# Kernel tuning notes

Hardware: AMD Instinct MI355X
Metric: run time of the kernel (lower is better)

The kernel has to match this reference:

```python
import jax, jax.numpy as jnp
import numpy as np
from itertools import permutations

NODE, BATCH, DIM, STEP = 32, 64, 32, 8
E = NODE * (NODE - 1)          # 992 directed edges (all ordered pairs)
K = 3                          # edge types
MSG_HID = 64; MSG_OUT = 64; N_HID = 64; PRED_LEN = 8


def setup_inputs() -> dict:
    key = jax.random.key(0)
    ks = jax.random.split(key, 12)
    es = jnp.asarray(np.array(list(permutations(range(NODE), 2))).T, dtype=jnp.int32)  # [2, E]
    x = jax.random.normal(ks[0], (BATCH, NODE, DIM, STEP), jnp.float32)
    z = jax.nn.softmax(jax.random.normal(ks[1], (BATCH, E, K), jnp.float32), axis=-1)
    p = lambda k, shape: jax.random.normal(k, shape, jnp.float32) * 0.1
    return dict(
        x=x, z=z, es=es,
        nodes_mask=jnp.zeros((NODE,), jnp.float32),
        edges_mask=jnp.zeros((E,), jnp.float32),
        mask=jnp.zeros((1,), jnp.float32),
        msg_W1=p(ks[2], (K, 2 * DIM, MSG_HID)), msg_b1=jnp.zeros((K, MSG_HID), jnp.float32),
        msg_W2=p(ks[3], (K, MSG_HID, MSG_OUT)), msg_b2=jnp.zeros((K, MSG_OUT), jnp.float32),
        out_W1=p(ks[4], (DIM + MSG_OUT, N_HID)), out_b1=jnp.zeros((N_HID,), jnp.float32),
        out_W2=p(ks[5], (N_HID, N_HID)), out_b2=jnp.zeros((N_HID,), jnp.float32),
        out_W3=p(ks[6], (N_HID, DIM)), out_b3=jnp.zeros((DIM,), jnp.float32),
        ge_Wi=p(ks[7], (3, N_HID, N_HID)), ge_bi=jnp.zeros((3, N_HID), jnp.float32),
        ge_Wh=p(ks[8], (3, N_HID, N_HID)), ge_bh=jnp.zeros((3, N_HID), jnp.float32),
        gn_Wi=p(ks[9], (3, N_HID + DIM, N_HID + DIM)), gn_bi=jnp.zeros((3, N_HID + DIM), jnp.float32),
        gn_Wh=p(ks[10], (3, N_HID + DIM, N_HID + DIM)), gn_bh=jnp.zeros((3, N_HID + DIM), jnp.float32),
    )


def _gru(inp, hid, Wi, bi, Wh, bh):
    # GRUX: state defaults to hidden
    r = jax.nn.sigmoid(inp @ Wi[0] + bi[0] + hid @ Wh[0] + bh[0])
    i = jax.nn.sigmoid(inp @ Wi[1] + bi[1] + hid @ Wh[1] + bh[1])
    n = jnp.tanh(inp @ Wi[2] + bi[2] + r * (hid @ Wh[2] + bh[2]))
    return (1.0 - i) * n + i * hid


def _run(x, z, es, msg_W1, msg_b1, msg_W2, msg_b2,
         out_W1, out_b1, out_W2, out_b2, out_W3, out_b3,
         ge_Wi, ge_bi, ge_Wh, ge_bh, gn_Wi, gn_bi, gn_Wh, gn_bh):
    xp = jnp.transpose(x, (1, 0, 3, 2))   # [node, batch, step, dim]
    zp = jnp.transpose(z, (1, 0, 2))      # [E, batch, K]
    col, row = es[0], es[1]               # 'o2i': col,row = es; aggregate at col
    counts = jnp.clip(jax.ops.segment_sum(jnp.ones((E,), x.dtype), col, num_segments=NODE), 1.0)
    h_node = h_edge = None
    x_m = None
    xs = []
    for t in range(STEP + PRED_LEN):
        x_in = xp[:, :, t, :] if t < STEP else x_m   # [node, batch, dim]
        # edge gather: msg = cat([x[row], x[col]])
        msg = jnp.concatenate([x_in[row], x_in[col]], axis=-1)  # [E, b, 2*dim]
        # per-edge-type 2-layer MLP mixture, weighted by z, normalized by K
        h1 = jax.nn.relu(jnp.einsum('ebi,kih->kebh', msg, msg_W1) + msg_b1[:, None, None, :])
        h2 = jax.nn.relu(jnp.einsum('kebh,kho->kebo', h1, msg_W2) + msg_b2[:, None, None, :])
        msgs = jnp.einsum('kebo,ebk->ebo', h2, zp) / K          # [E, b, msg_out]
        if h_edge is not None:
            msgs = _gru(msgs, h_edge, ge_Wi, ge_bi, ge_Wh, ge_bh)
        # scatter-mean to nodes
        agg = jax.ops.segment_sum(msgs, col, num_segments=NODE) / counts[:, None, None]
        cat = jnp.concatenate([x_in, agg], axis=-1)             # [node, b, dim+msg_out]
        if h_node is not None:
            cat = _gru(cat, h_node, gn_Wi, gn_bi, gn_Wh, gn_bh)
        h = jax.nn.relu(cat @ out_W1 + out_b1)
        h = jax.nn.relu(h @ out_W2 + out_b2)
        delta = h @ out_W3 + out_b3
        x_m = x_in + delta
        h_node, h_edge = cat, msgs
        xs.append(x_m)
    x_hat = jnp.transpose(jnp.stack(xs, axis=2), (1, 0, 3, 2))  # [batch, node, dim, T]
    return x_hat


def reference(x, z, es, nodes_mask, edges_mask, mask,
              msg_W1, msg_b1, msg_W2, msg_b2,
              out_W1, out_b1, out_W2, out_b2, out_W3, out_b3,
              ge_Wi, ge_bi, ge_Wh, ge_bh, gn_Wi, gn_bi, gn_Wh, gn_bh):
    x_hat = _run(x, z, es, msg_W1, msg_b1, msg_W2, msg_b2,
                 out_W1, out_b1, out_W2, out_b2, out_W3, out_b3,
                 ge_Wi, ge_bi, ge_Wh, ge_bh, gn_Wi, gn_bi, gn_Wh, gn_bh)
    return (x_hat[:, :, :, -PRED_LEN:], x_hat, x_hat)
```

## Files before the change

kernel.cpp:

```cpp
#include <hip/hip_runtime.h>
#include <hip/hip_bf16.h>

#define NNODE 32
#define NB    64
#define NDIM  32
#define NSTEP 8
#define NE    992
#define NTT   16

typedef __bf16 bf16;
typedef __attribute__((ext_vector_type(8))) __bf16 bf16x8;
typedef __attribute__((ext_vector_type(4))) __bf16 bf16x4;
typedef __attribute__((ext_vector_type(4))) float  f32x4;

__device__ __forceinline__ f32x4 mfma_bf16(bf16x8 a, bf16x8 b, f32x4 c) {
  return __builtin_amdgcn_mfma_f32_16x16x32_bf16(a, b, c, 0, 0, 0);
}
__device__ __forceinline__ float sigm(float x) { return 1.0f / (1.0f + __expf(-x)); }
__device__ __forceinline__ float tanh_f(float x) {
  x = fminf(fmaxf(x, -15.0f), 15.0f);
  float e = __expf(2.0f * x);
  return (e - 1.0f) / (e + 1.0f);
}

__global__ void prep_weights(
    const float* __restrict__ msgW1, const float* __restrict__ msgW2,
    const float* __restrict__ geWi,  const float* __restrict__ geWh,
    const float* __restrict__ gnWi,  const float* __restrict__ gnWh,
    const float* __restrict__ oW1,   const float* __restrict__ oW2,
    const float* __restrict__ oW3,
    bf16* __restrict__ B1, bf16* __restrict__ B2,
    bf16* __restrict__ GI, bf16* __restrict__ GH,
    bf16* __restrict__ GN,
    bf16* __restrict__ OW1s, bf16* __restrict__ OW2s, bf16* __restrict__ OW3s) {
  int u = blockIdx.x * 256 + threadIdx.x;
  if (u < 12288) {
    int k = u >> 12, i = (u >> 6) & 63, h = u & 63;
    int kf = i >> 5, quad = (i >> 3) & 3, j = i & 7;
    int nn = k * 64 + h, nt = nn >> 4, lane = quad * 16 + (nn & 15);
    int slot = ((nt * 2 + kf) * 64 + lane) * 8 + j;
    B1[slot] = (bf16)msgW1[u];
    GI[slot] = (bf16)geWi[u];
    GH[slot] = (bf16)geWh[u];
    int ntl = h >> 4, lane2 = quad * 16 + (h & 15);
    int slot2 = k * 4096 + ((ntl * 2 + kf) * 64 + lane2) * 8 + j;
    B2[slot2] = (bf16)msgW2[u];
  } else if (u < 39936) {
    int v = u - 12288;
    int kk = v / 9216, rem = v % 9216, i = rem / 96, h = rem % 96;
    int kf = i >> 5, loc = i & 31, quad = loc >> 3, j = loc & 7;
    int nn = kk * 96 + h, nt = nn >> 4, lane = quad * 16 + (nn & 15);
    int slot = ((nt * 3 + kf) * 64 + lane) * 8 + j;
    GN[slot]         = (bf16)gnWi[v];
    GN[27648 + slot] = (bf16)gnWh[v];
  } else if (u < 46080) {
    int v = u - 39936; int i = v >> 6, h = v & 63;
    int kf = i >> 5, loc = i & 31, quad = loc >> 3, j = loc & 7;
    int nt = h >> 4, lane = quad * 16 + (h & 15);
    OW1s[((nt * 3 + kf) * 64 + lane) * 8 + j] = (bf16)oW1[v];
  } else if (u < 50176) {
    int v = u - 46080; int i = v >> 6, h = v & 63;
    int kf = i >> 5, quad = (i >> 3) & 3, j = i & 7;
    int nt = h >> 4, lane = quad * 16 + (h & 15);
    OW2s[((nt * 2 + kf) * 64 + lane) * 8 + j] = (bf16)oW2[v];
  } else if (u < 52224) {
    int v = u - 50176; int i = v >> 5, h = v & 31;
    int kf = i >> 5, quad = (i >> 3) & 3, j = i & 7;
    int nt = h >> 4, lane = quad * 16 + (h & 15);
    OW3s[((nt * 2 + kf) * 64 + lane) * 8 + j] = (bf16)oW3[v];
  }
}

__global__ void copy_x(const float* __restrict__ x, float* __restrict__ xf,
                       bf16* __restrict__ xball) {
  int u = blockIdx.x * 256 + threadIdx.x;
  int n = u >> 11, b = (u >> 5) & 63, d = u & 31;
  int base = ((b * 32 + n) * 32 + d) * 8;
  xf[u] = x[base];
#pragma unroll
  for (int t = 0; t < 8; t++)
    xball[t * 65536 + u] = (bf16)x[base + t];
}

__device__ __forceinline__ void edge_body(
    char* smem, int e0, int tid,
    const bf16* __restrict__ xsrc, const int* __restrict__ es,
    const float* __restrict__ z,
    const bf16* __restrict__ B1, const bf16* __restrict__ B2,
    const float* __restrict__ mb1, const float* __restrict__ mb2,
    const bf16* __restrict__ GI, const bf16* __restrict__ GH,
    const float* __restrict__ gbi, const float* __restrict__ gbh,
    const bf16* __restrict__ hedR, bf16* __restrict__ hedW, int t) {
  char* scrbuf = smem;
  float (*zL)[64][3] = (float(*)[64][3])(smem + 51200);
  bf16 (*Hh)[64][72] = (bf16(*)[64][72])(smem + 52736);
  bf16 (*A)[64][72]   = (bf16(*)[64][72])scrbuf;
  bf16 (*A2)[64][200] = (bf16(*)[64][200])scrbuf;

  int c0_ = es[e0],     r0 = es[NE + e0];
  int c1_ = es[e0 + 1], r1 = es[NE + e0 + 1];
  int wv = tid >> 6, ln = tid & 63, quad = ln >> 4, l16 = ln & 15;
  int rg = wv & 3, cg = wv >> 2;
  int m = rg * 16 + l16;

  for (int u = tid; u < 384; u += 512) {
    int pe = u / 192, rem = u % 192, b = rem / 3, k = rem % 3;
    zL[pe][b][k] = z[(b * NE + e0 + pe) * 3 + k];
  }
  if (t > 0) {
    for (int u = tid; u < 1024; u += 512) {
      int pe = u >> 9, c = u & 511;
      int b = c >> 3, j = c & 7;
      *(bf16x8*)&Hh[pe][b][j * 8] =
          *(const bf16x8*)(hedR + (e0 + pe) * 4096 + b * 64 + j * 8);
    }
  }

  bf16x8 af[2][2];
  af[0][0] = *(const bf16x8*)(xsrc + r0 * 2048 + m * 32 + quad * 8);
  af[0][1] = *(const bf16x8*)(xsrc + c0_ * 2048 + m * 32 + quad * 8);
  af[1][0] = *(const bf16x8*)(xsrc + r1 * 2048 + m * 32 + quad * 8);
  af[1][1] = *(const bf16x8*)(xsrc + c1_ * 2048 + m * 32 + quad * 8);

  f32x4 acc1[2][6];
#pragma unroll
  for (int pe = 0; pe < 2; pe++)
#pragma unroll
    for (int q = 0; q < 6; q++) { f32x4 zz = {0.f,0.f,0.f,0.f}; acc1[pe][q] = zz; }
#pragma unroll
  for (int j = 0; j < 6; j++) {
    int nt = cg * 6 + j;
    bf16x8 w0 = *(const bf16x8*)&B1[(nt * 2 + 0) * 512 + ln * 8];
    bf16x8 w1 = *(const bf16x8*)&B1[(nt * 2 + 1) * 512 + ln * 8];
#pragma unroll
    for (int pe = 0; pe < 2; pe++) {
      acc1[pe][j] = mfma_bf16(af[pe][0], w0, acc1[pe][j]);
      acc1[pe][j] = mfma_bf16(af[pe][1], w1, acc1[pe][j]);
    }
  }
#pragma unroll
  for (int j = 0; j < 6; j++) {
    int nt = cg * 6 + j;
    int n = nt * 16 + l16;
    float bias = mb1[n];
#pragma unroll
    for (int pe = 0; pe < 2; pe++)
#pragma unroll
      for (int r = 0; r < 4; r++) {
        float v = acc1[pe][j][r] + bias;
        A2[pe][rg * 16 + quad * 4 + r][n] = (bf16)(v > 0.f ? v : 0.f);
      }
  }
  __syncthreads();
  f32x4 acc2[2][3][2];
#pragma unroll
  for (int pe = 0; pe < 2; pe++)
#pragma unroll
    for (int kt = 0; kt < 3; kt++)
#pragma unroll
      for (int oi = 0; oi < 2; oi++) { f32x4 zz = {0.f,0.f,0.f,0.f}; acc2[pe][kt][oi] = zz; }
#pragma unroll
  for (int kt = 0; kt < 3; kt++) {
    bf16x8 a2f[2][2];
#pragma unroll
    for (int pe = 0; pe < 2; pe++)
#pragma unroll
      for (int kf = 0; kf < 2; kf++)
        a2f[pe][kf] = *(const bf16x8*)&A2[pe][m][kt * 64 + kf * 32 + quad * 8];
#pragma unroll
    for (int oi = 0; oi < 2; oi++) {
      int ot = cg * 2 + oi;
      bf16x8 w0 = *(const bf16x8*)&B2[kt * 4096 + (ot * 2 + 0) * 512 + ln * 8];
      bf16x8 w1 = *(const bf16x8*)&B2[kt * 4096 + (ot * 2 + 1) * 512 + ln * 8];
#pragma unroll
      for (int pe = 0; pe < 2; pe++) {
        acc2[pe][kt][oi] = mfma_bf16(a2f[pe][0], w0, acc2[pe][kt][oi]);
        acc2[pe][kt][oi] = mfma_bf16(a2f[pe][1], w1, acc2[pe][kt][oi]);
      }
    }
  }
  __syncthreads();
  float mb2v[3][2];
#pragma unroll
  for (int kt = 0; kt < 3; kt++)
#pragma unroll
    for (int oi = 0; oi < 2; oi++)
      mb2v[kt][oi] = mb2[kt * 64 + (cg * 2 + oi) * 16 + l16];
#pragma unroll
  for (int pe = 0; pe < 2; pe++)
#pragma unroll
    for (int r = 0; r < 4; r++) {
      int b = rg * 16 + quad * 4 + r;
      float z0 = zL[pe][b][0], z1 = zL[pe][b][1], z2 = zL[pe][b][2];
#pragma unroll
      for (int oi = 0; oi < 2; oi++) {
        int o = (cg * 2 + oi) * 16 + l16;
        float h0 = acc2[pe][0][oi][r] + mb2v[0][oi]; h0 = h0 > 0.f ? h0 : 0.f;
        float h1 = acc2[pe][1][oi][r] + mb2v[1][oi]; h1 = h1 > 0.f ? h1 : 0.f;
        float h2 = acc2[pe][2][oi][r] + mb2v[2][oi]; h2 = h2 > 0.f ? h2 : 0.f;
        float val = (h0 * z0 + h1 * z1 + h2 * z2) * (1.0f / 3.0f);
        if (t == 0)
          hedW[(e0 + pe) * 4096 + b * 64 + o] = (bf16)val;
        else
          A[pe][b][o] = (bf16)val;
      }
    }
  if (t > 0) {
    __syncthreads();
    bf16x8 ai[2][2], ah[2][2];
#pragma unroll
    for (int pe = 0; pe < 2; pe++)
#pragma unroll
      for (int kf = 0; kf < 2; kf++) {
        ai[pe][kf] = *(const bf16x8*)&A[pe][m][kf * 32 + quad * 8];
        ah[pe][kf] = *(const bf16x8*)&Hh[pe][m][kf * 32 + quad * 8];
      }
#pragma unroll
    for (int oi = 0; oi < 2; oi++) {
      int ot = cg * 2 + oi;
      f32x4 gr[2], gi2[2], gni2[2], gnh2[2];
#pragma unroll
      for (int pe = 0; pe < 2; pe++) {
        f32x4 zz = {0.f,0.f,0.f,0.f};
        gr[pe] = zz; gi2[pe] = zz; gni2[pe] = zz; gnh2[pe] = zz;
      }
#pragma unroll
      for (int g = 0; g < 2; g++) {
        int nt = g * 4 + ot;
        bf16x8 wi0 = *(const bf16x8*)&GI[(nt * 2 + 0) * 512 + ln * 8];
        bf16x8 wi1 = *(const bf16x8*)&GI[(nt * 2 + 1) * 512 + ln * 8];
        bf16x8 wh0 = *(const bf16x8*)&GH[(nt * 2 + 0) * 512 + ln * 8];
        bf16x8 wh1 = *(const bf16x8*)&GH[(nt * 2 + 1) * 512 + ln * 8];
#pragma unroll
        for (int pe = 0; pe < 2; pe++) {
          f32x4 a = g ? gi2[pe] : gr[pe];
          a = mfma_bf16(ai[pe][0], wi0, a);
          a = mfma_bf16(ai[pe][1], wi1, a);
          a = mfma_bf16(ah[pe][0], wh0, a);
          a = mfma_bf16(ah[pe][1], wh1, a);
          if (g) gi2[pe] = a; else gr[pe] = a;
        }
      }
      {
        int nt = 8 + ot;
        bf16x8 wi0 = *(const bf16x8*)&GI[(nt * 2 + 0) * 512 + ln * 8];
        bf16x8 wi1 = *(const bf16x8*)&GI[(nt * 2 + 1) * 512 + ln * 8];
        bf16x8 wh0 = *(const bf16x8*)&GH[(nt * 2 + 0) * 512 + ln * 8];
        bf16x8 wh1 = *(const bf16x8*)&GH[(nt * 2 + 1) * 512 + ln * 8];
#pragma unroll
        for (int pe = 0; pe < 2; pe++) {
          gni2[pe] = mfma_bf16(ai[pe][0], wi0, gni2[pe]);
          gni2[pe] = mfma_bf16(ai[pe][1], wi1, gni2[pe]);
          gnh2[pe] = mfma_bf16(ah[pe][0], wh0, gnh2[pe]);
          gnh2[pe] = mfma_bf16(ah[pe][1], wh1, gnh2[pe]);
        }
      }
      int o = ot * 16 + l16;
      float bir = gbi[o],       bhr = gbh[o];
      float bii = gbi[64 + o],  bhi = gbh[64 + o];
      float bin = gbi[128 + o], bhn = gbh[128 + o];
#pragma unroll
      for (int pe = 0; pe < 2; pe++)
#pragma unroll
        for (int r = 0; r < 4; r++) {
          int b = rg * 16 + quad * 4 + r;
          float xr = gr[pe][r]   + bir + bhr;
          float xi = gi2[pe][r]  + bii + bhi;
          float xn = gni2[pe][r] + bin;
          float hn = gnh2[pe][r] + bhn;
          float rgt = sigm(xr);
          float ig  = sigm(xi);
          float ng  = tanh_f(xn + rgt * hn);
          float hv  = (float)Hh[pe][b][o];
          hedW[(e0 + pe) * 4096 + b * 64 + o] =
              (bf16)((1.0f - ig) * ng + ig * hv);
        }
    }
  }
}

__device__ __forceinline__ void node_body(
    char* smem, int nq, int tid,
    const float* __restrict__ x, const bf16* __restrict__ hed,
    float* __restrict__ xf, bf16* __restrict__ xb, float* __restrict__ hnode,
    const bf16* __restrict__ GN,
    const float* __restrict__ gnbi, const float* __restrict__ gnbh,
    const bf16* __restrict__ OW1, const float* __restrict__ ob1,
    const bf16* __restrict__ OW2, const float* __restrict__ ob2,
    const bf16* __restrict__ OW3, const float* __restrict__ ob3,
    float* __restrict__ out, int t) {
  float (*aggf)[64]      = (float(*)[64])(smem);
  float (*xinf)[32]      = (float(*)[32])(smem + 4096);
  float (*hvf)[96]       = (float(*)[96])(smem + 6144);
  bf16  (*c0b)[112]      = (bf16(*)[112])(smem + 12288);
  bf16  (*hvb)[112]      = (bf16(*)[112])(smem + 15872);
  float (*gsum)[16][290] = (float(*)[16][290])(smem + 19456);
  bf16  (*cnb)[112]      = (bf16(*)[112])(smem + 56576);
  bf16  (*s1b)[112]      = (bf16(*)[112])(smem + 60160);
  bf16  (*s2b)[112]      = (bf16(*)[112])(smem + 63744);
  int n = nq >> 2, q = nq & 3;
  int wv = tid >> 6, ln = tid & 63, quad = ln >> 4, l16 = ln & 15;
  if (tid < 256) {
    int r = tid >> 4, o4 = tid & 15;
    const bf16x4* bp = (const bf16x4*)hed + (size_t)n * 31 * 1024 + (q * 16 + r) * 16 + o4;
    float sx = 0.f, sy = 0.f, sz = 0.f, sw = 0.f;
#pragma unroll
    for (int e2 = 0; e2 < 31; e2++) {
      bf16x4 v = bp[e2 * 1024];
      sx += (float)v[0]; sy += (float)v[1]; sz += (float)v[2]; sw += (float)v[3];
    }
    const float inv = 1.0f / 31.0f;
    sx *= inv; sy *= inv; sz *= inv; sw *= inv;
    int o = o4 * 4;
    aggf[r][o] = sx; aggf[r][o + 1] = sy; aggf[r][o + 2] = sz; aggf[r][o + 3] = sw;
    c0b[r][32 + o] = (bf16)sx; c0b[r][33 + o] = (bf16)sy;
    c0b[r][34 + o] = (bf16)sz; c0b[r][35 + o] = (bf16)sw;
  }
  if (tid < 128) {
    int r = tid >> 3, d0 = (tid & 7) * 4;
    int b = q * 16 + r;
#pragma unroll
    for (int k = 0; k < 4; k++) {
      float v = xf[n * 2048 + b * 32 + d0 + k];
      xinf[r][d0 + k] = v;
      c0b[r][d0 + k] = (bf16)v;
    }
  }
  if (t > 0 && tid < 256) {
    int r = tid >> 4, cb = (tid & 15) * 6;
    int row = n * 64 + q * 16 + r;
#pragma unroll
    for (int k = 0; k < 6; k++) {
      float v = hnode[row * 96 + cb + k];
      hvf[r][cb + k] = v;
      hvb[r][cb + k] = (bf16)v;
    }
  }
  __syncthreads();
  if (t > 0 && wv < 4) {
    int mat = wv >> 1, sel = wv & 1;
    const bf16(*Ab)[112] = mat ? hvb : c0b;
    bf16x8 af[3];
#pragma unroll
    for (int kf = 0; kf < 3; kf++)
      af[kf] = *(const bf16x8*)&Ab[l16][kf * 32 + quad * 8];
    const bf16* W = GN + mat * 27648;
    f32x4 accn[9];
#pragma unroll
    for (int q2 = 0; q2 < 9; q2++) { f32x4 zz = {0.f,0.f,0.f,0.f}; accn[q2] = zz; }
#pragma unroll
    for (int nt2 = 0; nt2 < 9; nt2++) {
      int nt = sel * 9 + nt2;
#pragma unroll
      for (int kf = 0; kf < 3; kf++) {
        bf16x8 bfrag = *(const bf16x8*)&W[((nt * 3 + kf) * 64 + ln) * 8];
        accn[nt2] = mfma_bf16(af[kf], bfrag, accn[nt2]);
      }
    }
#pragma unroll
    for (int nt2 = 0; nt2 < 9; nt2++) {
      int col = (sel * 9 + nt2) * 16 + l16;
#pragma unroll
      for (int rr = 0; rr < 4; rr++)
        gsum[mat][quad * 4 + rr][col] = accn[nt2][rr];
    }
  }
  __syncthreads();
  if (tid < 256) {
    int r = tid >> 4, cb = (tid & 15) * 6;
    int row = n * 64 + q * 16 + r;
#pragma unroll
    for (int k = 0; k < 6; k++) {
      int c = cb + k;
      float v;
      if (t > 0) {
        float xr = gsum[0][r][c] + gnbi[c] + gsum[1][r][c] + gnbh[c];
        float xi = gsum[0][r][96 + c] + gnbi[96 + c] + gsum[1][r][96 + c] + gnbh[96 + c];
        float xn = gsum[0][r][192 + c] + gnbi[192 + c];
        float hn = gsum[1][r][192 + c] + gnbh[192 + c];
        float rg = sigm(xr);
        float ig = sigm(xi);
        float ng = tanh_f(xn + rg * hn);
        v = (1.0f - ig) * ng + ig * hvf[r][c];
      } else {
        v = (c < 32) ? xinf[r][c] : aggf[r][c - 32];
      }
      cnb[r][c] = (bf16)v;
      hnode[row * 96 + c] = v;
    }
  }
  __syncthreads();
  if (wv < 4) {
    bf16x8 af3[3];
#pragma unroll
    for (int kf = 0; kf < 3; kf++)
      af3[kf] = *(const bf16x8*)&cnb[l16][kf * 32 + quad * 8];
    f32x4 accn = {0.f, 0.f, 0.f, 0.f};
#pragma unroll
    for (int kf = 0; kf < 3; kf++) {
      bf16x8 bfrag = *(const bf16x8*)&OW1[((wv * 3 + kf) * 64 + ln) * 8];
      accn = mfma_bf16(af3[kf], bfrag, accn);
    }
    int col = wv * 16 + l16;
    float bias = ob1[col];
#pragma unroll
    for (int rr = 0; rr < 4; rr++) {
      float vv = accn[rr] + bias;
      s1b[quad * 4 + rr][col] = (bf16)(vv > 0.f ? vv : 0.f);
    }
  }
  __syncthreads();
  if (wv < 4) {
    bf16x8 af2[2];
#pragma unroll
    for (int kf = 0; kf < 2; kf++)
      af2[kf] = *(const bf16x8*)&s1b[l16][kf * 32 + quad * 8];
    f32x4 accn = {0.f, 0.f, 0.f, 0.f};
#pragma unroll
    for (int kf = 0; kf < 2; kf++) {
      bf16x8 bfrag = *(const bf16x8*)&OW2[((wv * 2 + kf) * 64 + ln) * 8];
      accn = mfma_bf16(af2[kf], bfrag, accn);
    }
    int col = wv * 16 + l16;
    float bias = ob2[col];
#pragma unroll
    for (int rr = 0; rr < 4; rr++) {
      float vv = accn[rr] + bias;
      s2b[quad * 4 + rr][col] = (bf16)(vv > 0.f ? vv : 0.f);
    }
  }
  __syncthreads();
  if (wv < 2) {
    bf16x8 af2[2];
#pragma unroll
    for (int kf = 0; kf < 2; kf++)
      af2[kf] = *(const bf16x8*)&s2b[l16][kf * 32 + quad * 8];
    f32x4 accn = {0.f, 0.f, 0.f, 0.f};
#pragma unroll
    for (int kf = 0; kf < 2; kf++) {
      bf16x8 bfrag = *(const bf16x8*)&OW3[((wv * 2 + kf) * 64 + ln) * 8];
      accn = mfma_bf16(af2[kf], bfrag, accn);
    }
    int d = wv * 16 + l16;
    float bias = ob3[d];
#pragma unroll
    for (int rr = 0; rr < 4; rr++) {
      int r = quad * 4 + rr;
      int b = q * 16 + r;
      float xm = xinf[r][d] + accn[rr] + bias;
      int base = (b * 32 + n) * 32 + d;
      out[524288 + base * 16 + t] = xm;
      out[1572864 + base * 16 + t] = xm;
      if (t >= NSTEP) out[base * 8 + (t - NSTEP)] = xm;
      float vnext = (t + 1 < NSTEP) ? x[base * 8 + (t + 1)] : xm;
      xf[n * 2048 + b * 32 + d] = vnext;
      xb[n * 2048 + b * 32 + d] = (bf16)vnext;
    }
  }
}

__global__ __launch_bounds__(512, 4) void edge_step(
    const bf16* __restrict__ xsrc, const int* __restrict__ es,
    const float* __restrict__ z,
    const bf16* __restrict__ B1, const bf16* __restrict__ B2,
    const float* __restrict__ mb1, const float* __restrict__ mb2,
    const bf16* __restrict__ GI, const bf16* __restrict__ GH,
    const float* __restrict__ gbi, const float* __restrict__ gbh,
    const bf16* __restrict__ hedR, bf16* __restrict__ hedW, int t) {
  __shared__ __align__(16) char smem[71168];
  edge_body(smem, blockIdx.x * 2, threadIdx.x, xsrc, es, z, B1, B2, mb1, mb2,
            GI, GH, gbi, gbh, hedR, hedW, t);
}

__global__ __launch_bounds__(256) void node_kernel(
    const float* __restrict__ x, const bf16* __restrict__ hed,
    float* __restrict__ xf, bf16* __restrict__ xb, float* __restrict__ hnode,
    const bf16* __restrict__ GN,
    const float* __restrict__ gnbi, const float* __restrict__ gnbh,
    const bf16* __restrict__ OW1, const float* __restrict__ ob1,
    const bf16* __restrict__ OW2, const float* __restrict__ ob2,
    const bf16* __restrict__ OW3, const float* __restrict__ ob3,
    float* __restrict__ out, int t) {
  __shared__ __align__(16) char smem[67328];
  node_body(smem, blockIdx.x, threadIdx.x, x, hed, xf, xb, hnode, GN,
            gnbi, gnbh, OW1, ob1, OW2, ob2, OW3, ob3, out, t);
}

__global__ __launch_bounds__(512, 4) void fused_ne(
    const float* __restrict__ x,
    const bf16* __restrict__ xsrc, const int* __restrict__ es,
    const float* __restrict__ z,
    const bf16* __restrict__ B1, const bf16* __restrict__ B2,
    const float* __restrict__ mb1, const float* __restrict__ mb2,
    const bf16* __restrict__ GI, const bf16* __restrict__ GH,
    const float* __restrict__ gbi, const float* __restrict__ gbh,
    const bf16* __restrict__ hedR, bf16* __restrict__ hedW,
    float* __restrict__ xf, bf16* __restrict__ xb, float* __restrict__ hnode,
    const bf16* __restrict__ GN,
    const float* __restrict__ gnbi, const float* __restrict__ gnbh,
    const bf16* __restrict__ OW1, const float* __restrict__ ob1,
    const bf16* __restrict__ OW2, const float* __restrict__ ob2,
    const bf16* __restrict__ OW3, const float* __restrict__ ob3,
    float* __restrict__ out, int te) {
  __shared__ __align__(16) char smem[71168];
  if (blockIdx.x < 128) {
    node_body(smem, blockIdx.x, threadIdx.x, x, hedR, xf, xb, hnode, GN,
              gnbi, gnbh, OW1, ob1, OW2, ob2, OW3, ob3, out, te - 1);
  } else {
    edge_body(smem, (blockIdx.x - 128) * 2, threadIdx.x, xsrc, es, z, B1, B2,
              mb1, mb2, GI, GH, gbi, gbh, hedR, hedW, te);
  }
}

extern "C" void kernel_launch(void* const* d_in, const int* in_sizes, int n_in,
                              void* d_out, int out_size, void* d_ws, size_t ws_size,
                              hipStream_t stream) {
  const float* x     = (const float*)d_in[0];
  const float* z     = (const float*)d_in[1];
  const int*   es    = (const int*)d_in[2];
  const float* msgW1 = (const float*)d_in[6];
  const float* msgb1 = (const float*)d_in[7];
  const float* msgW2 = (const float*)d_in[8];
  const float* msgb2 = (const float*)d_in[9];
  const float* oW1   = (const float*)d_in[10];
  const float* ob1   = (const float*)d_in[11];
  const float* oW2   = (const float*)d_in[12];
  const float* ob2   = (const float*)d_in[13];
  const float* oW3   = (const float*)d_in[14];
  const float* ob3   = (const float*)d_in[15];
  const float* geWi  = (const float*)d_in[16];
  const float* gebi  = (const float*)d_in[17];
  const float* geWh  = (const float*)d_in[18];
  const float* gebh  = (const float*)d_in[19];
  const float* gnWi  = (const float*)d_in[20];
  const float* gnbi  = (const float*)d_in[21];
  const float* gnWh  = (const float*)d_in[22];
  const float* gnbh  = (const float*)d_in[23];
  float* out = (float*)d_out;

  char* p = (char*)d_ws;
  bf16*  hedA  = (bf16*)p;   p += (size_t)NE * 4096 * 2;
  bf16*  hedB  = (bf16*)p;   p += (size_t)NE * 4096 * 2;
  bf16*  xball = (bf16*)p;   p += (size_t)8 * 65536 * 2;
  float* xf    = (float*)p;  p += 65536 * 4;
  bf16*  xb    = (bf16*)p;   p += 65536 * 2;
  float* hnode = (float*)p;  p += 196608 * 4;
  bf16*  B1sw  = (bf16*)p;   p += 12288 * 2;
  bf16*  B2sw  = (bf16*)p;   p += 12288 * 2;
  bf16*  GIsw  = (bf16*)p;   p += 12288 * 2;
  bf16*  GHsw  = (bf16*)p;   p += 12288 * 2;
  bf16*  GNsw  = (bf16*)p;   p += 55296 * 2;
  bf16*  OW1s  = (bf16*)p;   p += 6144 * 2;
  bf16*  OW2s  = (bf16*)p;   p += 4096 * 2;
  bf16*  OW3s  = (bf16*)p;   p += 2048 * 2;

  bf16* hbuf[2] = {hedA, hedB};

  prep_weights<<<204, 256, 0, stream>>>(msgW1, msgW2, geWi, geWh, gnWi, gnWh,
                                        oW1, oW2, oW3,
                                        B1sw, B2sw, GIsw, GHsw, GNsw,
                                        OW1s, OW2s, OW3s);
  copy_x<<<256, 256, 0, stream>>>(x, xf, xball);

  edge_step<<<NE / 2, 512, 0, stream>>>(xball, es, z, B1sw, B2sw, msgb1, msgb2,
                                        GIsw, GHsw, gebi, gebh,
                                        hbuf[1], hbuf[0], 0);
  for (int t = 1; t < NSTEP; t++) {
    fused_ne<<<128 + NE / 2, 512, 0, stream>>>(
        x, xball + (size_t)t * 65536, es, z, B1sw, B2sw, msgb1, msgb2,
        GIsw, GHsw, gebi, gebh,
        hbuf[(t - 1) & 1], hbuf[t & 1],
        xf, xb, hnode, GNsw, gnbi, gnbh,
        OW1s, ob1, OW2s, ob2, OW3s, ob3, out, t);
  }
  node_kernel<<<128, 256, 0, stream>>>(x, hbuf[(NSTEP - 1) & 1], xf, xb, hnode,
                                       GNsw, gnbi, gnbh, OW1s, ob1, OW2s, ob2,
                                       OW3s, ob3, out, NSTEP - 1);
  for (int t = NSTEP; t < NTT; t++) {
    edge_step<<<NE / 2, 512, 0, stream>>>(xb, es, z, B1sw, B2sw, msgb1, msgb2,
                                          GIsw, GHsw, gebi, gebh,
                                          hbuf[(t - 1) & 1], hbuf[t & 1], t);
    node_kernel<<<128, 256, 0, stream>>>(x, hbuf[t & 1], xf, xb, hnode,
                                         GNsw, gnbi, gnbh, OW1s, ob1, OW2s, ob2,
                                         OW3s, ob3, out, t);
  }
}
```

Baseline: 553.5 us.

## Fuse autoregressive node and edge steps with a global spin-flag dependency

In the autoregressive phase (t>=NSTEP), each step previously launched an edge kernel and then a node kernel, which serialized them. Now node and edge work for consecutive steps share one launch. Edge blocks prefetch their z and hidden-state data, then spin on a global counter until all 128 node blocks for the step have published xb. This hides launch gaps and overlaps edge prefetch with node compute. It risks deadlock if edge blocks fill the GPU before the node blocks get scheduled, and spinning blocks hold CU resources.

After: 1.781 ms. +221.7%, slower.

```diff
diff --git a/kernel.cpp b/kernel.cpp
--- a/kernel.cpp
+++ b/kernel.cpp
@@ -72,8 +72,9 @@
 }
 
 __global__ void copy_x(const float* __restrict__ x, float* __restrict__ xf,
-                       bf16* __restrict__ xball) {
+                       bf16* __restrict__ xball, unsigned* __restrict__ flag) {
   int u = blockIdx.x * 256 + threadIdx.x;
+  if (u == 0) flag[0] = 0u;
   int n = u >> 11, b = (u >> 5) & 63, d = u & 31;
   int base = ((b * 32 + n) * 32 + d) * 8;
   xf[u] = x[base];
@@ -90,7 +91,8 @@
     const float* __restrict__ mb1, const float* __restrict__ mb2,
     const bf16* __restrict__ GI, const bf16* __restrict__ GH,
     const float* __restrict__ gbi, const float* __restrict__ gbh,
-    const bf16* __restrict__ hedR, bf16* __restrict__ hedW, int t) {
+    const bf16* __restrict__ hedR, bf16* __restrict__ hedW,
+    const unsigned* __restrict__ flag, unsigned target, int t) {
   char* scrbuf = smem;
   float (*zL)[64][3] = (float(*)[64][3])(smem + 51200);
   bf16 (*Hh)[64][72] = (bf16(*)[64][72])(smem + 52736);
@@ -114,6 +116,14 @@
       *(bf16x8*)&Hh[pe][b][j * 8] =
           *(const bf16x8*)(hedR + (e0 + pe) * 4096 + b * 64 + j * 8);
     }
+  }
+  if (target) {
+    if (tid == 0) {
+      while (__hip_atomic_load(flag, __ATOMIC_ACQUIRE, __HIP_MEMORY_SCOPE_AGENT) < target)
+        __builtin_amdgcn_s_sleep(8);
+    }
+    __syncthreads();
+    __threadfence();
   }
 
   bf16x8 af[2][2];
@@ -469,7 +479,7 @@
     const bf16* __restrict__ hedR, bf16* __restrict__ hedW, int t) {
   __shared__ __align__(16) char smem[71168];
   edge_body(smem, blockIdx.x * 2, threadIdx.x, xsrc, es, z, B1, B2, mb1, mb2,
-            GI, GH, gbi, gbh, hedR, hedW, t);
+            GI, GH, gbi, gbh, hedR, hedW, nullptr, 0u, t);
 }
 
 __global__ __launch_bounds__(256) void node_kernel(
@@ -508,7 +518,38 @@
               gnbi, gnbh, OW1, ob1, OW2, ob2, OW3, ob3, out, te - 1);
   } else {
     edge_body(smem, (blockIdx.x - 128) * 2, threadIdx.x, xsrc, es, z, B1, B2,
-              mb1, mb2, GI, GH, gbi, gbh, hedR, hedW, te);
+              mb1, mb2, GI, GH, gbi, gbh, hedR, hedW, nullptr, 0u, te);
+  }
+}
+
+__global__ __launch_bounds__(512, 4) void fused_spin(
+    const float* __restrict__ x, const int* __restrict__ es,
+    const float* __restrict__ z,
+    const bf16* __restrict__ B1, const bf16* __restrict__ B2,
+    const float* __restrict__ mb1, const float* __restrict__ mb2,
+    const bf16* __restrict__ GI, const bf16* __restrict__ GH,
+    const float* __restrict__ gbi, const float* __restrict__ gbh,
+    const bf16* __restrict__ hedR, bf16* __restrict__ hedW,
+    float* __restrict__ xf, bf16* __restrict__ xb, float* __restrict__ hnode,
+    const bf16* __restrict__ GN,
+    const float* __restrict__ gnbi, const float* __restrict__ gnbh,
+    const bf16* __restrict__ OW1, const float* __restrict__ ob1,
+    const bf16* __restrict__ OW2, const float* __restrict__ ob2,
+    const bf16* __restrict__ OW3, const float* __restrict__ ob3,
+    float* __restrict__ out,
+    unsigned* __restrict__ flag, unsigned target, int tn) {
+  __shared__ __align__(16) char smem[71168];
+  if (blockIdx.x < 128) {
+    node_body(smem, blockIdx.x, threadIdx.x, x, hedR, xf, xb, hnode, GN,
+              gnbi, gnbh, OW1, ob1, OW2, ob2, OW3, ob3, out, tn);
+    __syncthreads();
+    if (threadIdx.x == 0) {
+      __threadfence();
+      __hip_atomic_fetch_add(flag, 1u, __ATOMIC_RELEASE, __HIP_MEMORY_SCOPE_AGENT);
+    }
+  } else {
+    edge_body(smem, (blockIdx.x - 128) * 2, threadIdx.x, xb, es, z, B1, B2,
+              mb1, mb2, GI, GH, gbi, gbh, hedR, hedW, flag, target, tn + 1);
   }
 }
 
@@ -553,6 +594,7 @@
   bf16*  OW1s  = (bf16*)p;   p += 6144 * 2;
   bf16*  OW2s  = (bf16*)p;   p += 4096 * 2;
   bf16*  OW3s  = (bf16*)p;   p += 2048 * 2;
+  unsigned* flag = (unsigned*)p; p += 16;
 
   bf16* hbuf[2] = {hedA, hedB};
 
@@ -560,7 +602,7 @@
                                         oW1, oW2, oW3,
                                         B1sw, B2sw, GIsw, GHsw, GNsw,
                                         OW1s, OW2s, OW3s);
-  copy_x<<<256, 256, 0, stream>>>(x, xf, xball);
+  copy_x<<<256, 256, 0, stream>>>(x, xf, xball, flag);
 
   edge_step<<<NE / 2, 512, 0, stream>>>(xball, es, z, B1sw, B2sw, msgb1, msgb2,
                                         GIsw, GHsw, gebi, gebh,
@@ -573,15 +615,17 @@
         xf, xb, hnode, GNsw, gnbi, gnbh,
         OW1s, ob1, OW2s, ob2, OW3s, ob3, out, t);
   }
-  node_kernel<<<128, 256, 0, stream>>>(x, hbuf[(NSTEP - 1) & 1], xf, xb, hnode,
+  for (int k = 0; k < 8; k++) {
+    int tn = NSTEP - 1 + k;
+    fused_spin<<<128 + NE / 2, 512, 0, stream>>>(
+        x, es, z, B1sw, B2sw, msgb1, msgb2,
+        GIsw, GHsw, gebi, gebh,
+        hbuf[tn & 1], hbuf[(tn + 1) & 1],
+        xf, xb, hnode, GNsw, gnbi, gnbh,
+        OW1s, ob1, OW2s, ob2, OW3s, ob3, out,
+        flag, (unsigned)((k + 1) * 128), tn);
+  }
+  node_kernel<<<128, 256, 0, stream>>>(x, hbuf[(NTT - 1) & 1], xf, xb, hnode,
                                        GNsw, gnbi, gnbh, OW1s, ob1, OW2s, ob2,
-                                       OW3s, ob3, out, NSTEP - 1);
-  for (int t = NSTEP; t < NTT; t++) {
-    edge_step<<<NE / 2, 512, 0, stream>>>(xb, es, z, B1sw, B2sw, msgb1, msgb2,
-                                          GIsw, GHsw, gebi, gebh,
-                                          hbuf[(t - 1) & 1], hbuf[t & 1], t);
-    node_kernel<<<128, 256, 0, stream>>>(x, hbuf[t & 1], xf, xb, hnode,
-                                         GNsw, gnbi, gnbh, OW1s, ob1, OW2s, ob2,
-                                         OW3s, ob3, out, t);
-  }
-}
+                                       OW3s, ob3, out, NTT - 1);
+}
```

## Fuse node GRU gate matmuls with elementwise epilogue in registers, drop gsum smem

Applied to the files above, without the earlier changes.

The node GRU now has six waves, each owning one 16-column tile and computing the r, i and n gate products for both input and hidden in registers. The gate nonlinearity is applied straight from the accumulators, so the large gsum shared-memory staging buffer and one barrier go away. Node kernel shared memory drops substantially and the block grows to 384 threads. The fused_ne kernel also calls node_body with 512 threads, and its smem layout and thread mapping must match. That is a correctness and occupancy risk there.

Result: faster. 532.7 us, median of 2 (-3.7%).

```diff
diff --git a/kernel.cpp b/kernel.cpp
--- a/kernel.cpp
+++ b/kernel.cpp
@@ -289,15 +289,14 @@
     const bf16* __restrict__ OW2, const float* __restrict__ ob2,
     const bf16* __restrict__ OW3, const float* __restrict__ ob3,
     float* __restrict__ out, int t) {
-  float (*aggf)[64]      = (float(*)[64])(smem);
-  float (*xinf)[32]      = (float(*)[32])(smem + 4096);
-  float (*hvf)[96]       = (float(*)[96])(smem + 6144);
-  bf16  (*c0b)[112]      = (bf16(*)[112])(smem + 12288);
-  bf16  (*hvb)[112]      = (bf16(*)[112])(smem + 15872);
-  float (*gsum)[16][290] = (float(*)[16][290])(smem + 19456);
-  bf16  (*cnb)[112]      = (bf16(*)[112])(smem + 56576);
-  bf16  (*s1b)[112]      = (bf16(*)[112])(smem + 60160);
-  bf16  (*s2b)[112]      = (bf16(*)[112])(smem + 63744);
+  float (*aggf)[64] = (float(*)[64])(smem);
+  float (*xinf)[32] = (float(*)[32])(smem + 4096);
+  float (*hvf)[96]  = (float(*)[96])(smem + 6144);
+  bf16  (*c0b)[112] = (bf16(*)[112])(smem + 12288);
+  bf16  (*hvb)[112] = (bf16(*)[112])(smem + 15872);
+  bf16  (*cnb)[112] = (bf16(*)[112])(smem + 19456);
+  bf16  (*s1b)[112] = (bf16(*)[112])(smem + 23040);
+  bf16  (*s2b)[112] = (bf16(*)[112])(smem + 26624);
   int n = nq >> 2, q = nq & 3;
   int wv = tid >> 6, ln = tid & 63, quad = ln >> 4, l16 = ln & 15;
   if (tid < 256) {
@@ -337,54 +336,58 @@
     }
   }
   __syncthreads();
-  if (t > 0 && wv < 4) {
-    int mat = wv >> 1, sel = wv & 1;
-    const bf16(*Ab)[112] = mat ? hvb : c0b;
-    bf16x8 af[3];
-#pragma unroll
-    for (int kf = 0; kf < 3; kf++)
-      af[kf] = *(const bf16x8*)&Ab[l16][kf * 32 + quad * 8];
-    const bf16* W = GN + mat * 27648;
-    f32x4 accn[9];
-#pragma unroll
-    for (int q2 = 0; q2 < 9; q2++) { f32x4 zz = {0.f,0.f,0.f,0.f}; accn[q2] = zz; }
-#pragma unroll
-    for (int nt2 = 0; nt2 < 9; nt2++) {
-      int nt = sel * 9 + nt2;
-#pragma unroll
-      for (int kf = 0; kf < 3; kf++) {
-        bf16x8 bfrag = *(const bf16x8*)&W[((nt * 3 + kf) * 64 + ln) * 8];
-        accn[nt2] = mfma_bf16(af[kf], bfrag, accn[nt2]);
-      }
-    }
-#pragma unroll
-    for (int nt2 = 0; nt2 < 9; nt2++) {
-      int col = (sel * 9 + nt2) * 16 + l16;
-#pragma unroll
-      for (int rr = 0; rr < 4; rr++)
-        gsum[mat][quad * 4 + rr][col] = accn[nt2][rr];
-    }
-  }
-  __syncthreads();
-  if (tid < 256) {
+  if (t > 0 && wv < 6) {
+    int ct = wv;
+    bf16x8 a0[3], a1[3];
+#pragma unroll
+    for (int kf = 0; kf < 3; kf++) {
+      a0[kf] = *(const bf16x8*)&c0b[l16][kf * 32 + quad * 8];
+      a1[kf] = *(const bf16x8*)&hvb[l16][kf * 32 + quad * 8];
+    }
+    const bf16* W0 = GN;
+    const bf16* W1 = GN + 27648;
+    f32x4 aR = {0.f,0.f,0.f,0.f}, bR = {0.f,0.f,0.f,0.f};
+    f32x4 aI = {0.f,0.f,0.f,0.f}, bI = {0.f,0.f,0.f,0.f};
+    f32x4 aN = {0.f,0.f,0.f,0.f}, bN = {0.f,0.f,0.f,0.f};
+#pragma unroll
+    for (int kf = 0; kf < 3; kf++) {
+      int ir = ((ct * 3 + kf) * 64 + ln) * 8;
+      int ii = (((6 + ct) * 3 + kf) * 64 + ln) * 8;
+      int in_ = (((12 + ct) * 3 + kf) * 64 + ln) * 8;
+      aR = mfma_bf16(a0[kf], *(const bf16x8*)&W0[ir],  aR);
+      bR = mfma_bf16(a1[kf], *(const bf16x8*)&W1[ir],  bR);
+      aI = mfma_bf16(a0[kf], *(const bf16x8*)&W0[ii],  aI);
+      bI = mfma_bf16(a1[kf], *(const bf16x8*)&W1[ii],  bI);
+      aN = mfma_bf16(a0[kf], *(const bf16x8*)&W0[in_], aN);
+      bN = mfma_bf16(a1[kf], *(const bf16x8*)&W1[in_], bN);
+    }
+    int col = ct * 16 + l16;
+    float bRc = gnbi[col] + gnbh[col];
+    float bIc = gnbi[96 + col] + gnbh[96 + col];
+    float bN0 = gnbi[192 + col], bN1 = gnbh[192 + col];
+    int rowbase = n * 64 + q * 16;
+#pragma unroll
+    for (int rr = 0; rr < 4; rr++) {
+      int row = quad * 4 + rr;
+      float xr = aR[rr] + bR[rr] + bRc;
+      float xi = aI[rr] + bI[rr] + bIc;
+      float xn = aN[rr] + bN0;
+      float hn = bN[rr] + bN1;
+      float rg = sigm(xr);
+      float ig = sigm(xi);
+      float ng = tanh_f(xn + rg * hn);
+      float v = (1.0f - ig) * ng + ig * hvf[row][col];
+      cnb[row][col] = (bf16)v;
+      hnode[(rowbase + row) * 96 + col] = v;
+    }
+  }
+  if (t == 0 && tid < 256) {
     int r = tid >> 4, cb = (tid & 15) * 6;
     int row = n * 64 + q * 16 + r;
 #pragma unroll
     for (int k = 0; k < 6; k++) {
       int c = cb + k;
-      float v;
-      if (t > 0) {
-        float xr = gsum[0][r][c] + gnbi[c] + gsum[1][r][c] + gnbh[c];
-        float xi = gsum[0][r][96 + c] + gnbi[96 + c] + gsum[1][r][96 + c] + gnbh[96 + c];
-        float xn = gsum[0][r][192 + c] + gnbi[192 + c];
-        float hn = gsum[1][r][192 + c] + gnbh[192 + c];
-        float rg = sigm(xr);
-        float ig = sigm(xi);
-        float ng = tanh_f(xn + rg * hn);
-        v = (1.0f - ig) * ng + ig * hvf[r][c];
-      } else {
-        v = (c < 32) ? xinf[r][c] : aggf[r][c - 32];
-      }
+      float v = (c < 32) ? xinf[r][c] : aggf[r][c - 32];
       cnb[r][c] = (bf16)v;
       hnode[row * 96 + c] = v;
     }
@@ -472,7 +475,7 @@
             GI, GH, gbi, gbh, hedR, hedW, t);
 }
 
-__global__ __launch_bounds__(256) void node_kernel(
+__global__ __launch_bounds__(384) void node_kernel(
     const float* __restrict__ x, const bf16* __restrict__ hed,
     float* __restrict__ xf, bf16* __restrict__ xb, float* __restrict__ hnode,
     const bf16* __restrict__ GN,
@@ -481,7 +484,7 @@
     const bf16* __restrict__ OW2, const float* __restrict__ ob2,
     const bf16* __restrict__ OW3, const float* __restrict__ ob3,
     float* __restrict__ out, int t) {
-  __shared__ __align__(16) char smem[67328];
+  __shared__ __align__(16) char smem[30208];
   node_body(smem, blockIdx.x, threadIdx.x, x, hed, xf, xb, hnode, GN,
             gnbi, gnbh, OW1, ob1, OW2, ob2, OW3, ob3, out, t);
 }
@@ -573,14 +576,14 @@
         xf, xb, hnode, GNsw, gnbi, gnbh,
         OW1s, ob1, OW2s, ob2, OW3s, ob3, out, t);
   }
-  node_kernel<<<128, 256, 0, stream>>>(x, hbuf[(NSTEP - 1) & 1], xf, xb, hnode,
+  node_kernel<<<128, 384, 0, stream>>>(x, hbuf[(NSTEP - 1) & 1], xf, xb, hnode,
                                        GNsw, gnbi, gnbh, OW1s, ob1, OW2s, ob2,
                                        OW3s, ob3, out, NSTEP - 1);
   for (int t = NSTEP; t < NTT; t++) {
     edge_step<<<NE / 2, 512, 0, stream>>>(xb, es, z, B1sw, B2sw, msgb1, msgb2,
                                           GIsw, GHsw, gebi, gebh,
                                           hbuf[(t - 1) & 1], hbuf[t & 1], t);
-    node_kernel<<<128, 256, 0, stream>>>(x, hbuf[t & 1], xf, xb, hnode,
+    node_kernel<<<128, 384, 0, stream>>>(x, hbuf[t & 1], xf, xb, hnode,
                                          GNsw, gnbi, gnbh, OW1s, ob1, OW2s, ob2,
                                          OW3s, ob3, out, t);
   }
```
